# Optimization experiments

Hardware: AMD Instinct MI355X
Metric: run time of the kernel (lower is better)

## Reference

```python
import jax, jax.numpy as jnp
import numpy as np
from jax import lax

B, L, D, DM, S, M, P = 8, 2048, 512, 1024, 32, 4, 4096


def setup_inputs() -> dict:
    key = jax.random.key(0)
    ks = jax.random.split(key, 13)
    emb = jax.random.normal(ks[0], (B, L, D), jnp.float32)
    pos = jax.random.randint(ks[1], (B, L), 1, P + 1)          # pos >= 1 (0 reserved for CLS)
    sid = jax.random.randint(ks[2], (B, L), 0, S)
    mod = jax.random.randint(ks[3], (B, L), 0, M)
    role = jax.random.randint(ks[4], (B, L), 0, 3)
    padding_mask = jax.random.uniform(ks[5], (B, L)) < 0.9
    W_proj = jax.random.normal(ks[6], (S, DM, D), jnp.float32) / np.float32(np.sqrt(D))
    b_proj = jax.random.normal(ks[7], (S, DM), jnp.float32) * 0.01
    cls_content = jax.random.normal(ks[8], (DM,), jnp.float32)
    pos_emb = jax.random.normal(ks[9], (P + 1, DM), jnp.float32) * 0.02
    id_emb = jax.random.normal(ks[10], (S + 1, DM), jnp.float32) * 0.02
    mod_emb = jax.random.normal(ks[11], (M, DM), jnp.float32) * 0.02
    role_emb = jax.random.normal(ks[12], (3, DM), jnp.float32) * 0.02
    return dict(emb=emb, pos=pos, sid=sid, mod=mod, role=role, padding_mask=padding_mask,
                W_proj=W_proj, b_proj=b_proj, cls_content=cls_content,
                pos_emb=pos_emb, id_emb=id_emb, mod_emb=mod_emb, role_emb=role_emb)


def _moe_project(emb, sid, padding_mask, W_proj, b_proj):
    """Per-token per-signal Linear: tokens[b,l] = W_proj[sid[b,l]] @ emb[b,l] + b_proj[sid[b,l]].
    Computed as S dense GEMMs masked per token (dense-dispatch MoE), avoiding an
    O(B*L*DM*D) gathered-weight tensor."""
    def step(acc, sWb):
        s, W, b = sWb
        y = jnp.einsum('bld,od->blo', emb, W) + b  # (B, L, DM)
        m = (sid == s) & padding_mask              # padded tokens stay zero
        return acc + jnp.where(m[..., None], y, 0.0), None
    acc0 = jnp.zeros(emb.shape[:2] + (W_proj.shape[1],), emb.dtype)
    acc, _ = lax.scan(step, acc0, (jnp.arange(W_proj.shape[0]), W_proj, b_proj))
    return acc


def reference(emb, pos, sid, mod, role, padding_mask,
              W_proj, b_proj, cls_content, pos_emb, id_emb, mod_emb, role_emb):
    Bc, Lc = pos.shape
    dm = cls_content.shape[0]
    cls_id = id_emb.shape[0] - 1  # == num_signals

    proj = _moe_project(emb, sid, padding_mask, W_proj, b_proj)  # (B, L, DM)

    cls = jnp.broadcast_to(cls_content, (Bc, 1, dm))
    tokens = jnp.concatenate([cls, proj], axis=1)                # (B, L+1, DM)

    pos_full = jnp.concatenate([jnp.zeros((Bc, 1), pos.dtype), pos], axis=1)
    sid_full = jnp.concatenate([jnp.full((Bc, 1), cls_id, sid.dtype), sid], axis=1)
    tokens = tokens + pos_emb[pos_full] + id_emb[sid_full]

    # modality + role embeddings only on non-CLS tokens (added even where padded, as in torch)
    tokens = tokens.at[:, 1:, :].add(mod_emb[mod] + role_emb[role])

    attn_keep = jnp.concatenate([jnp.ones((Bc, 1), bool), padding_mask], axis=1)
    return tokens, attn_keep
```

## Files before the change

kernel.cpp:

```cpp
#include <hip/hip_runtime.h>
#include <hip/hip_bf16.h>


#define NB   8
#define NL   2048
#define ND   512
#define NDM  1024
#define NS   32
#define NTOK (NB * NL)
#define LP1  (NL + 1)
#define MAXTILES 160
#define EXP_CAP 1024

static __device__ __forceinline__ size_t attn_off() { return (size_t)NB * LP1 * NDM; }

typedef __attribute__((ext_vector_type(8))) short bf16x8;
typedef __attribute__((ext_vector_type(4))) float f32x4;

__device__ __forceinline__ unsigned short f2bf(float f) {
    unsigned int x = __float_as_uint(f);
    x += 0x7fffu + ((x >> 16) & 1u);
    return (unsigned short)(x >> 16);
}

__device__ __forceinline__ float bf2f(unsigned short s) {
    return __uint_as_float(((unsigned int)s) << 16);
}

__device__ __forceinline__ bf16x8 cvt8(float4 a, float4 b) {
    bf16x8 r;
    r[0] = (short)__bfloat16_as_ushort(__float2bfloat16(a.x));
    r[1] = (short)__bfloat16_as_ushort(__float2bfloat16(a.y));
    r[2] = (short)__bfloat16_as_ushort(__float2bfloat16(a.z));
    r[3] = (short)__bfloat16_as_ushort(__float2bfloat16(a.w));
    r[4] = (short)__bfloat16_as_ushort(__float2bfloat16(b.x));
    r[5] = (short)__bfloat16_as_ushort(__float2bfloat16(b.y));
    r[6] = (short)__bfloat16_as_ushort(__float2bfloat16(b.z));
    r[7] = (short)__bfloat16_as_ushort(__float2bfloat16(b.w));
    return r;
}

__device__ __forceinline__ float4 ld4(const float* p) { return *(const float4*)p; }
__device__ __forceinline__ float4 add4(float4 a, float4 b) {
    return make_float4(a.x + b.x, a.y + b.y, a.z + b.z, a.w + b.w);
}

__global__ void k_bucket(const int* __restrict__ sid, const int* __restrict__ mask,
                         int* __restrict__ cnt, int* __restrict__ kidx,
                         int* __restrict__ tokList, float* __restrict__ out) {
    int t = blockIdx.x * 256 + threadIdx.x;
    if (t >= NTOK) return;
    int s = sid[t];
    bool keep = mask[t] != 0;
    int b = t >> 11, l = t & (NL - 1);
    out[attn_off() + (size_t)b * LP1 + l + 1] = keep ? 1.0f : 0.0f;
    if (t < NB) out[attn_off() + (size_t)t * LP1] = 1.0f;
    int ki = -1;
    if (keep) {
        ki = atomicAdd(&cnt[s], 1);
        if (ki < EXP_CAP) tokList[s * EXP_CAP + ki] = t;
    }
    kidx[t] = ki;
}

__global__ void k_tiles(const int* __restrict__ cnt, int* __restrict__ meta,
                        int* __restrict__ bOff, int4* __restrict__ tiles,
                        const float* __restrict__ me, const float* __restrict__ re,
                        float* __restrict__ mrT) {
    if (threadIdx.x == 0) {
        int idx = 0, cbase = 0;
        for (int e = 0; e < NS; ++e) {
            int c = min(cnt[e], EXP_CAP);
            bOff[e] = cbase;
            for (int r = 0; r < c; r += 128)
                tiles[idx++] = make_int4(e, r, min(128, c - r), cbase + r);
            cbase += c;
        }
        meta[0] = idx;
    }
    for (int i = threadIdx.x; i < 12 * (NDM / 4); i += 256) {
        int mr = i / (NDM / 4); int o = (i % (NDM / 4)) * 4;
        int m = mr / 3, ro = mr % 3;
        float4 v = add4(ld4(me + (size_t)m * NDM + o), ld4(re + (size_t)ro * NDM + o));
        *(float4*)&mrT[(size_t)mr * NDM + o] = v;
    }
}

__global__ __launch_bounds__(256) void k_gemm(
    const float* __restrict__ emb, const float* __restrict__ Wp,
    const int* __restrict__ tokList, const int4* __restrict__ tiles,
    const int* __restrict__ meta, unsigned short* __restrict__ projC) {
    if (blockIdx.y >= meta[0]) return;
    int4 td = tiles[blockIdx.y];
    const int e = td.x, rowBase = td.y, nRows = td.z, cBase = td.w;
    const int nBase = blockIdx.x * 128;

    __shared__ short SA[2][128 * 32];
    __shared__ short SB[2][128 * 32];

    const int tid  = threadIdx.x;
    const int lane = tid & 63;
    const int w    = tid >> 6;
    const int wr   = w >> 1, wc = w & 1;
    const int fr   = lane & 15, kg = lane >> 4;

    const int srow = tid >> 2;
    const int sch  = tid & 3;
    const size_t eBase = (size_t)e * EXP_CAP + rowBase;
    int ar0 = (srow < nRows) ? srow : 0;
    int ar1 = (srow + 64 < nRows) ? srow + 64 : 0;
    int tok0 = tokList[eBase + ar0];
    int tok1 = tokList[eBase + ar1];
    const float* a0 = emb + (size_t)tok0 * ND + sch * 8;
    const float* a1 = emb + (size_t)tok1 * ND + sch * 8;
    const float* b0 = Wp + ((size_t)e * NDM + nBase + srow) * ND + sch * 8;
    const float* b1 = Wp + ((size_t)e * NDM + nBase + srow + 64) * ND + sch * 8;
    const int wo0 = srow * 32 + (sch ^ ((srow >> 1) & 3)) * 8;
    const int wo1 = wo0 + 64 * 32;

    f32x4 acc[4][4];
#pragma unroll
    for (int i = 0; i < 4; ++i)
#pragma unroll
        for (int j = 0; j < 4; ++j)
            acc[i][j] = (f32x4){0.f, 0.f, 0.f, 0.f};

    float4 ta0a, ta0b, ta1a, ta1b, tb0a, tb0b, tb1a, tb1b;
    bf16x8 na0, na1, nb0, nb1;

#define LDF(ks) do {                                           \
        ta0a = ld4(a0 + (ks) * 32); ta0b = ld4(a0 + (ks) * 32 + 4); \
        ta1a = ld4(a1 + (ks) * 32); ta1b = ld4(a1 + (ks) * 32 + 4); \
        tb0a = ld4(b0 + (ks) * 32); tb0b = ld4(b0 + (ks) * 32 + 4); \
        tb1a = ld4(b1 + (ks) * 32); tb1b = ld4(b1 + (ks) * 32 + 4); \
    } while (0)
#define CVT() do {                                             \
        na0 = cvt8(ta0a, ta0b); na1 = cvt8(ta1a, ta1b);        \
        nb0 = cvt8(tb0a, tb0b); nb1 = cvt8(tb1a, tb1b);        \
    } while (0)

    LDF(0); CVT();
    *(bf16x8*)&SA[0][wo0] = na0;
    *(bf16x8*)&SA[0][wo1] = na1;
    *(bf16x8*)&SB[0][wo0] = nb0;
    *(bf16x8*)&SB[0][wo1] = nb1;
    LDF(1); CVT();

    const int pc = kg ^ ((fr >> 1) & 3);
    for (int ks = 0; ks < ND / 32; ++ks) {
        const int cur = ks & 1;
        __syncthreads();
        if (ks < ND / 32 - 1) {
            *(bf16x8*)&SA[cur ^ 1][wo0] = na0;
            *(bf16x8*)&SA[cur ^ 1][wo1] = na1;
            *(bf16x8*)&SB[cur ^ 1][wo0] = nb0;
            *(bf16x8*)&SB[cur ^ 1][wo1] = nb1;
        }
        if (ks < ND / 32 - 2) LDF(ks + 2);
        bf16x8 af[4], bv[4];
#pragma unroll
        for (int i = 0; i < 4; ++i)
            af[i] = *(const bf16x8*)&SA[cur][(wr * 64 + i * 16 + fr) * 32 + pc * 8];
#pragma unroll
        for (int j = 0; j < 4; ++j)
            bv[j] = *(const bf16x8*)&SB[cur][(wc * 64 + j * 16 + fr) * 32 + pc * 8];
#pragma unroll
        for (int i = 0; i < 4; ++i)
#pragma unroll
            for (int j = 0; j < 4; ++j)
                acc[i][j] = __builtin_amdgcn_mfma_f32_16x16x32_bf16(af[i], bv[j], acc[i][j], 0, 0, 0);
        if (ks < ND / 32 - 2) CVT();
    }
#undef LDF
#undef CVT

#pragma unroll
    for (int i = 0; i < 4; ++i) {
#pragma unroll
        for (int r = 0; r < 4; ++r) {
            int row = wr * 64 + i * 16 + kg * 4 + r;
            if (row < nRows) {
                size_t crow = (size_t)(cBase + row) * NDM + nBase;
#pragma unroll
                for (int j = 0; j < 4; ++j)
                    projC[crow + wc * 64 + j * 16 + fr] = f2bf(acc[i][j][r]);
            }
        }
    }
}

__global__ void k_out(const int* __restrict__ pos, const int* __restrict__ sid,
                      const int* __restrict__ mod, const int* __restrict__ role,
                      const int* __restrict__ mask, const int* __restrict__ kidx,
                      const int* __restrict__ bOff,
                      const float* __restrict__ bp, const float* __restrict__ cls_c,
                      const float* __restrict__ pe, const float* __restrict__ ie,
                      const float* __restrict__ mrT,
                      const unsigned short* __restrict__ projC,
                      float* __restrict__ out) {
    int l1 = blockIdx.x;
    int b  = blockIdx.y;
    int o  = threadIdx.x * 4;
    float4 v;
    if (l1 == 0) {
        v = add4(add4(ld4(cls_c + o), ld4(pe + o)), ld4(ie + (size_t)NS * NDM + o));
    } else {
        int t = b * NL + l1 - 1;
        int p = pos[t], s = sid[t], mr = mod[t] * 3 + role[t];
        v = add4(ld4(pe + (size_t)p * NDM + o), ld4(ie + (size_t)s * NDM + o));
        v = add4(v, ld4(mrT + (size_t)mr * NDM + o));
        if (mask[t] != 0) {
            v = add4(v, ld4(bp + (size_t)s * NDM + o));
            int ki = kidx[t];
            if (ki >= 0 && ki < EXP_CAP) {
                const unsigned short* pr = projC + (size_t)(bOff[s] + ki) * NDM + o;
                v.x += bf2f(pr[0]); v.y += bf2f(pr[1]);
                v.z += bf2f(pr[2]); v.w += bf2f(pr[3]);
            }
        }
    }
    *(float4*)&out[((size_t)b * LP1 + l1) * NDM + o] = v;
}

extern "C" void kernel_launch(void* const* d_in, const int* in_sizes, int n_in,
                              void* d_out, int out_size, void* d_ws, size_t ws_size,
                              hipStream_t stream) {
    const float* emb  = (const float*)d_in[0];
    const int* pos    = (const int*)d_in[1];
    const int* sid    = (const int*)d_in[2];
    const int* mod    = (const int*)d_in[3];
    const int* role   = (const int*)d_in[4];
    const int* mask   = (const int*)d_in[5];
    const float* Wp   = (const float*)d_in[6];
    const float* bp   = (const float*)d_in[7];
    const float* cls  = (const float*)d_in[8];
    const float* pe   = (const float*)d_in[9];
    const float* ie   = (const float*)d_in[10];
    const float* me   = (const float*)d_in[11];
    const float* re   = (const float*)d_in[12];
    float* out = (float*)d_out;

    int* ws        = (int*)d_ws;
    int* cnt       = ws;
    int* meta      = ws + 32;
    int* bOff      = ws + 64;
    int4* tiles    = (int4*)(ws + 128);
    int* tokList   = ws + 1024;
    int* kidx      = ws + 33792;
    float* mrT     = (float*)(ws + 50176);
    unsigned short* projC = (unsigned short*)((char*)d_ws + 262144);

    hipMemsetAsync(ws, 0, 64 * sizeof(int), stream);
    k_bucket<<<NTOK / 256, 256, 0, stream>>>(sid, mask, cnt, kidx, tokList, out);
    k_tiles<<<1, 256, 0, stream>>>(cnt, meta, bOff, tiles, me, re, mrT);

    dim3 gg(NDM / 128, MAXTILES);
    k_gemm<<<gg, 256, 0, stream>>>(emb, Wp, tokList, tiles, meta, projC);

    dim3 go(LP1, NB);
    k_out<<<go, 256, 0, stream>>>(pos, sid, mod, role, mask, kidx, bOff,
                                  bp, cls, pe, ie, mrT, projC, out);
}
```

Baseline: 132.7 us.

## Drop tile-planning kernel, derive tiles in GEMM, widen output kernel rows

The single-thread k_tiles kernel is removed. The modality+role table build moves into k_bucket, and each GEMM block derives its expert, row range and compacted offset by scanning the per-expert counts itself. The output kernel now handles two rows per block with eight elements per thread, and computes each expert's base offset from counts held in shared memory. This is meant to cut one launch and a serial planning step from the critical path, at the cost of redundant 32-step scans in every GEMM block and prefix loops in the output kernel.

```diff
diff --git a/kernel.cpp b/kernel.cpp
--- a/kernel.cpp
+++ b/kernel.cpp
@@ -46,41 +46,28 @@
 }
 
 __global__ void k_bucket(const int* __restrict__ sid, const int* __restrict__ mask,
+                         const int* __restrict__ mod, const int* __restrict__ role,
+                         const float* __restrict__ me, const float* __restrict__ re,
                          int* __restrict__ cnt, int* __restrict__ kidx,
-                         int* __restrict__ tokList, float* __restrict__ out) {
+                         int* __restrict__ tokList, float* __restrict__ mrT,
+                         float* __restrict__ out) {
     int t = blockIdx.x * 256 + threadIdx.x;
-    if (t >= NTOK) return;
-    int s = sid[t];
-    bool keep = mask[t] != 0;
-    int b = t >> 11, l = t & (NL - 1);
-    out[attn_off() + (size_t)b * LP1 + l + 1] = keep ? 1.0f : 0.0f;
-    if (t < NB) out[attn_off() + (size_t)t * LP1] = 1.0f;
-    int ki = -1;
-    if (keep) {
-        ki = atomicAdd(&cnt[s], 1);
-        if (ki < EXP_CAP) tokList[s * EXP_CAP + ki] = t;
-    }
-    kidx[t] = ki;
-}
-
-__global__ void k_tiles(const int* __restrict__ cnt, int* __restrict__ meta,
-                        int* __restrict__ bOff, int4* __restrict__ tiles,
-                        const float* __restrict__ me, const float* __restrict__ re,
-                        float* __restrict__ mrT) {
-    if (threadIdx.x == 0) {
-        int idx = 0, cbase = 0;
-        for (int e = 0; e < NS; ++e) {
-            int c = min(cnt[e], EXP_CAP);
-            bOff[e] = cbase;
-            for (int r = 0; r < c; r += 128)
-                tiles[idx++] = make_int4(e, r, min(128, c - r), cbase + r);
-            cbase += c;
-        }
-        meta[0] = idx;
-    }
-    for (int i = threadIdx.x; i < 12 * (NDM / 4); i += 256) {
-        int mr = i / (NDM / 4); int o = (i % (NDM / 4)) * 4;
-        int m = mr / 3, ro = mr % 3;
+    if (t < NTOK) {
+        int s = sid[t];
+        bool keep = mask[t] != 0;
+        int b = t >> 11, l = t & (NL - 1);
+        out[attn_off() + (size_t)b * LP1 + l + 1] = keep ? 1.0f : 0.0f;
+        if (t < NB) out[attn_off() + (size_t)t * LP1] = 1.0f;
+        int ki = -1;
+        if (keep) {
+            ki = atomicAdd(&cnt[s], 1);
+            if (ki < EXP_CAP) tokList[s * EXP_CAP + ki] = t;
+        }
+        kidx[t] = ki;
+    }
+    if (blockIdx.x < 12) {
+        int mr = blockIdx.x, m = mr / 3, ro = mr % 3;
+        int o = threadIdx.x * 4;
         float4 v = add4(ld4(me + (size_t)m * NDM + o), ld4(re + (size_t)ro * NDM + o));
         *(float4*)&mrT[(size_t)mr * NDM + o] = v;
     }
@@ -88,11 +75,22 @@
 
 __global__ __launch_bounds__(256) void k_gemm(
     const float* __restrict__ emb, const float* __restrict__ Wp,
-    const int* __restrict__ tokList, const int4* __restrict__ tiles,
-    const int* __restrict__ meta, unsigned short* __restrict__ projC) {
-    if (blockIdx.y >= meta[0]) return;
-    int4 td = tiles[blockIdx.y];
-    const int e = td.x, rowBase = td.y, nRows = td.z, cBase = td.w;
+    const int* __restrict__ tokList, const int* __restrict__ cnt,
+    unsigned short* __restrict__ projC) {
+    int e = -1, rowBase = 0, nRows = 0, cBase = 0;
+    {
+        int T = blockIdx.y, idx = 0, cb = 0;
+        for (int s = 0; s < NS; ++s) {
+            int c = min(cnt[s], EXP_CAP);
+            int nt = (c + 127) >> 7;
+            if (T >= idx && T < idx + nt) {
+                e = s; rowBase = (T - idx) * 128;
+                nRows = min(128, c - rowBase); cBase = cb + rowBase;
+            }
+            idx += nt; cb += c;
+        }
+        if (e < 0) return;
+    }
     const int nBase = blockIdx.x * 128;
 
     __shared__ short SA[2][128 * 32];
@@ -192,34 +190,52 @@
 __global__ void k_out(const int* __restrict__ pos, const int* __restrict__ sid,
                       const int* __restrict__ mod, const int* __restrict__ role,
                       const int* __restrict__ mask, const int* __restrict__ kidx,
-                      const int* __restrict__ bOff,
+                      const int* __restrict__ cnt,
                       const float* __restrict__ bp, const float* __restrict__ cls_c,
                       const float* __restrict__ pe, const float* __restrict__ ie,
                       const float* __restrict__ mrT,
                       const unsigned short* __restrict__ projC,
                       float* __restrict__ out) {
-    int l1 = blockIdx.x;
+    __shared__ int scnt[NS];
+    if (threadIdx.x < NS) scnt[threadIdx.x] = min(cnt[threadIdx.x], EXP_CAP);
+    __syncthreads();
+    int rp = threadIdx.x >> 7;
+    int o  = (threadIdx.x & 127) * 8;
+    int l1 = blockIdx.x * 2 + rp;
     int b  = blockIdx.y;
-    int o  = threadIdx.x * 4;
-    float4 v;
+    if (l1 > NL) return;
+    float4 v0, v1;
     if (l1 == 0) {
-        v = add4(add4(ld4(cls_c + o), ld4(pe + o)), ld4(ie + (size_t)NS * NDM + o));
+        const float* ieC = ie + (size_t)NS * NDM;
+        v0 = add4(add4(ld4(cls_c + o), ld4(pe + o)), ld4(ieC + o));
+        v1 = add4(add4(ld4(cls_c + o + 4), ld4(pe + o + 4)), ld4(ieC + o + 4));
     } else {
         int t = b * NL + l1 - 1;
         int p = pos[t], s = sid[t], mr = mod[t] * 3 + role[t];
-        v = add4(ld4(pe + (size_t)p * NDM + o), ld4(ie + (size_t)s * NDM + o));
-        v = add4(v, ld4(mrT + (size_t)mr * NDM + o));
+        const float* peR = pe + (size_t)p * NDM + o;
+        const float* ieR = ie + (size_t)s * NDM + o;
+        const float* mrR = mrT + (size_t)mr * NDM + o;
+        v0 = add4(add4(ld4(peR), ld4(ieR)), ld4(mrR));
+        v1 = add4(add4(ld4(peR + 4), ld4(ieR + 4)), ld4(mrR + 4));
         if (mask[t] != 0) {
-            v = add4(v, ld4(bp + (size_t)s * NDM + o));
+            const float* bpR = bp + (size_t)s * NDM + o;
+            v0 = add4(v0, ld4(bpR));
+            v1 = add4(v1, ld4(bpR + 4));
             int ki = kidx[t];
             if (ki >= 0 && ki < EXP_CAP) {
-                const unsigned short* pr = projC + (size_t)(bOff[s] + ki) * NDM + o;
-                v.x += bf2f(pr[0]); v.y += bf2f(pr[1]);
-                v.z += bf2f(pr[2]); v.w += bf2f(pr[3]);
+                int boff = 0;
+                for (int q = 0; q < s; ++q) boff += scnt[q];
+                const unsigned short* pr = projC + (size_t)(boff + ki) * NDM + o;
+                v0.x += bf2f(pr[0]); v0.y += bf2f(pr[1]);
+                v0.z += bf2f(pr[2]); v0.w += bf2f(pr[3]);
+                v1.x += bf2f(pr[4]); v1.y += bf2f(pr[5]);
+                v1.z += bf2f(pr[6]); v1.w += bf2f(pr[7]);
             }
         }
     }
-    *(float4*)&out[((size_t)b * LP1 + l1) * NDM + o] = v;
+    float* dst = &out[((size_t)b * LP1 + l1) * NDM + o];
+    *(float4*)dst = v0;
+    *(float4*)(dst + 4) = v1;
 }
 
 extern "C" void kernel_launch(void* const* d_in, const int* in_sizes, int n_in,
@@ -242,22 +258,19 @@
 
     int* ws        = (int*)d_ws;
     int* cnt       = ws;
-    int* meta      = ws + 32;
-    int* bOff      = ws + 64;
-    int4* tiles    = (int4*)(ws + 128);
     int* tokList   = ws + 1024;
     int* kidx      = ws + 33792;
     float* mrT     = (float*)(ws + 50176);
     unsigned short* projC = (unsigned short*)((char*)d_ws + 262144);
 
-    hipMemsetAsync(ws, 0, 64 * sizeof(int), stream);
-    k_bucket<<<NTOK / 256, 256, 0, stream>>>(sid, mask, cnt, kidx, tokList, out);
-    k_tiles<<<1, 256, 0, stream>>>(cnt, meta, bOff, tiles, me, re, mrT);
+    hipMemsetAsync(cnt, 0, 32 * sizeof(int), stream);
+    k_bucket<<<NTOK / 256, 256, 0, stream>>>(sid, mask, mod, role, me, re,
+                                             cnt, kidx, tokList, mrT, out);
 
     dim3 gg(NDM / 128, MAXTILES);
-    k_gemm<<<gg, 256, 0, stream>>>(emb, Wp, tokList, tiles, meta, projC);
-
-    dim3 go(LP1, NB);
-    k_out<<<go, 256, 0, stream>>>(pos, sid, mod, role, mask, kidx, bOff,
+    k_gemm<<<gg, 256, 0, stream>>>(emb, Wp, tokList, cnt, projC);
+
+    dim3 go((LP1 + 1) / 2, NB);
+    k_out<<<go, 256, 0, stream>>>(pos, sid, mod, role, mask, kidx, cnt,
                                   bp, cls, pe, ie, mrT, projC, out);
 }
```

Result: faster. 122.6 us (-7.6%).
